# Optimization experiments

Measured on AMD Instinct MI355X. Metric: run time of the kernel, lower is better.

Reference implementation:

```python
import jax, jax.numpy as jnp
import numpy as np

B = 8
RESOLUTIONS = [65, 129, 257, 513, 1025]
NUM_POINTS = [0, 4096, 16384, 65536, 262144]
CLIP_MIN = -1e9
FINAL = 1025          # last resolution (both axes)
B_MIN, B_MAX = -1.0, 1.0
BALANCE = 0.5


def setup_inputs() -> dict:
    key = jax.random.key(0)
    k1, k2, k3, k4 = jax.random.split(key, 4)
    return {
        "w1": jax.random.normal(k1, (2, 256), jnp.float32),
        "b1": jax.random.normal(k2, (256,), jnp.float32),
        "w2": jax.random.normal(k3, (256, 1), jnp.float32),
        "b2": jax.random.normal(k4, (1,), jnp.float32),
    }


def _interp_bilinear_ac(x, H, W):
    """F.interpolate(..., mode='bilinear', align_corners=True). x: [B, C, h, w]."""
    b, c, h, w = x.shape
    ys = jnp.linspace(0.0, h - 1.0, H)
    xs = jnp.linspace(0.0, w - 1.0, W)
    y0 = jnp.floor(ys).astype(jnp.int32)
    y1 = jnp.minimum(y0 + 1, h - 1)
    wy = ys - y0
    x0 = jnp.floor(xs).astype(jnp.int32)
    x1 = jnp.minimum(x0 + 1, w - 1)
    wx = xs - x0
    # interpolate rows, then columns
    top = x[:, :, y0, :] * (1.0 - wy)[None, None, :, None] + x[:, :, y1, :] * wy[None, None, :, None]
    return top[:, :, :, x0] * (1.0 - wx) + top[:, :, :, x1] * wx


def _batch_eval(coords, w1, b1, w2, b2):
    """coords: [B, N, 2] in final-resolution pixel space (align_corners=False mapping).
    Returns occupancy [B, N] (C == 1)."""
    coords2d = coords / FINAL + 0.5 / FINAL                 # normalize to [0, 1]
    p = coords2d * (B_MAX - B_MIN) + B_MIN                  # [B, N, 2] in world coords
    h = jax.nn.relu(jnp.einsum('bnd,dh->bnh', p, w1) + b1)  # [B, N, 256]
    occ = jax.nn.sigmoid(jnp.einsum('bnh,ho->bno', h, w2) + b2)
    return occ[..., 0]


def reference(w1, b1, w2, b2):
    occ = None
    for i, res in enumerate(RESOLUTIONS):
        if i == 0:
            # init_coords: grid of res x res points spanning [0, FINAL-1]
            xs = jnp.linspace(0.0, FINAL - 1.0, res)
            gy, gx = jnp.meshgrid(xs, xs, indexing='ij')          # y rows, x cols
            coords = jnp.stack([gx.ravel(), gy.ravel()], axis=-1)  # [N, 2] (x, y)
            coords = jnp.broadcast_to(coords, (B, res * res, 2))
            o = _batch_eval(coords, w1, b1, w2, b2)               # [B, N]
            occ = o.reshape(B, 1, res, res)                       # [B, C, H, W]
        else:
            occ = _interp_bilinear_ac(occ, res, res)
            npt = NUM_POINTS[i]
            if npt <= 0:
                continue
            # uncertainty = -|occ - balance_value|
            unc = -jnp.abs(occ - BALANCE)                          # [B, 1, H, W]
            flat_unc = unc.reshape(B, res * res)
            scores, idx = jax.lax.top_k(flat_unc, npt)             # [B, npt]
            px = (idx % res).astype(jnp.float32)
            py = (idx // res).astype(jnp.float32)
            stride = (FINAL - 1.0) / (res - 1.0)
            coords = jnp.stack([px, py], axis=-1) * stride         # [B, npt, 2]
            new_vals = _batch_eval(coords, w1, b1, w2, b2)         # [B, npt]
            occ_flat = occ.reshape(B, res * res)
            old_vals = jnp.take_along_axis(occ_flat, idx, axis=1)
            vals = jnp.where(scores >= CLIP_MIN, new_vals, old_vals)
            occ_flat = jax.vmap(lambda o, i2, v: o.at[i2].set(v))(occ_flat, idx, vals)
            occ = occ_flat.reshape(B, 1, res, res)
    return occ
```

## Files before the change

### kernel.cpp

```cpp
#include <hip/hip_runtime.h>
#include <stdint.h>

#define HID 256
#define NMAXPIX (1025 * 1025)
#define NREP 8
#define NSEG 2048

#define HISTA_OFF 0
#define HISTB_OFF 16384
#define HISTC_OFF 32768
#define SCAL_OFF  40960
#define TIC_OFF   41024
#define STAGE_U32 43072

__device__ __forceinline__ unsigned long long aload64(const unsigned long long* p) {
    return __hip_atomic_load(p, __ATOMIC_RELAXED, __HIP_MEMORY_SCOPE_AGENT);
}
__device__ __forceinline__ void astore64(unsigned long long* p, unsigned long long v) {
    __hip_atomic_store(p, v, __ATOMIC_RELAXED, __HIP_MEMORY_SCOPE_AGENT);
}

__device__ __forceinline__ float mlp_eval4(float wx, float wy,
                                           const float4* __restrict__ w1x,
                                           const float4* __restrict__ w1y,
                                           const float4* __restrict__ vb1,
                                           const float4* __restrict__ vw2, float b2v) {
    const float C0 = (float)(0.5 / 1025.0);
    float px = (wx / 1025.0f + C0) * 2.0f - 1.0f;
    float py = (wy / 1025.0f + C0) * 2.0f - 1.0f;
    float a0 = 0.f, a1 = 0.f, a2 = 0.f, a3 = 0.f;
#pragma unroll 8
    for (int q = 0; q < HID / 4; ++q) {
        float4 a = w1x[q], b = w1y[q], c = vb1[q], d = vw2[q];
        float h0 = px * a.x + py * b.x + c.x;
        float h1 = px * a.y + py * b.y + c.y;
        float h2 = px * a.z + py * b.z + c.z;
        float h3 = px * a.w + py * b.w + c.w;
        h0 = h0 > 0.f ? h0 : 0.f;
        h1 = h1 > 0.f ? h1 : 0.f;
        h2 = h2 > 0.f ? h2 : 0.f;
        h3 = h3 > 0.f ? h3 : 0.f;
        a0 += h0 * d.x;
        a1 += h1 * d.y;
        a2 += h2 * d.z;
        a3 += h3 * d.w;
    }
    float x = ((a0 + a1) + (a2 + a3)) + b2v;
    float r;
    if (x >= 0.f) { r = 1.0f / (1.0f + expf(-x)); }
    else { float e = expf(x); r = e / (1.0f + e); }
    return r;
}

__device__ __forceinline__ uint32_t block_exscan_256(uint32_t v, volatile uint32_t* lds4) {
    int lane = threadIdx.x & 63, w = threadIdx.x >> 6;
    uint32_t inc = v;
#pragma unroll
    for (int d = 1; d < 64; d <<= 1) {
        uint32_t o = (uint32_t)__shfl_up((int)inc, d, 64);
        if (lane >= d) inc += o;
    }
    if (lane == 63) lds4[w] = inc;
    __syncthreads();
    uint32_t woff = 0;
    for (int i = 0; i < w; ++i) woff += lds4[i];
    return woff + inc - v;
}

__device__ void scan_generic(const uint32_t* __restrict__ hist, int NB, int nrep,
                             uint32_t rem_in, uint32_t prefix_in, int shift,
                             uint32_t* outp, uint32_t* outr,
                             volatile uint32_t* lds4, volatile uint32_t* ldspair) {
    int tid = threadIdx.x;
    int C = NB >> 8;
    int b0 = NB - (tid + 1) * C;
    uint32_t cnts[8];
#pragma unroll
    for (int k = 0; k < 8; ++k) cnts[k] = 0;
    for (int rep = 0; rep < nrep; ++rep) {
        const uint4* p = (const uint4*)(hist + (size_t)rep * NB + b0);
#pragma unroll
        for (int g = 0; g < 2; ++g) {
            if (g * 4 < C) {
                uint4 v = p[g];
                cnts[g * 4 + 0] += v.x;
                cnts[g * 4 + 1] += v.y;
                cnts[g * 4 + 2] += v.z;
                cnts[g * 4 + 3] += v.w;
            }
        }
    }
    uint32_t ssum = 0;
    for (int k = 0; k < C; ++k) ssum += cnts[k];
    uint32_t excl = block_exscan_256(ssum, lds4);
    uint32_t run = excl;
    for (int k = 0; k < C; ++k) {
        uint32_t c = cnts[C - 1 - k];
        if (rem_in > run && rem_in <= run + c) {
            ldspair[0] = (prefix_in << shift) | (uint32_t)(b0 + C - 1 - k);
            ldspair[1] = rem_in - run;
        }
        run += c;
    }
    __syncthreads();
    *outp = ldspair[0];
    *outr = ldspair[1];
}

__device__ __forceinline__ void hist_add(uint32_t* lh, uint32_t bin, bool act, int lane) {
    unsigned long long m = __ballot(act);
    if (m) {
        int leader = __ffsll(m) - 1;
        uint32_t lbin = (uint32_t)__shfl((int)bin, leader, 64);
        unsigned long long smk = __ballot(act && bin == lbin);
        if (smk == m) {
            if (lane == leader) atomicAdd(&lh[lbin], (uint32_t)__popcll(m));
        } else if (act) {
            atomicAdd(&lh[bin], 1u);
        }
    }
}

__device__ __forceinline__ float up2x(const float* __restrict__ in, int rp, int r, int n) {
    int i = n / r, j = n % r;
    int i2 = i >> 1, j2 = j >> 1;
    float v;
    if ((i & 1) == 0) {
        if ((j & 1) == 0) {
            v = in[i2 * rp + j2];
        } else {
            float a = in[i2 * rp + j2], b = in[i2 * rp + j2 + 1];
            v = a * 0.5f + b * 0.5f;
        }
    } else {
        if ((j & 1) == 0) {
            float a = in[i2 * rp + j2], b = in[(i2 + 1) * rp + j2];
            v = a * 0.5f + b * 0.5f;
        } else {
            float a = in[i2 * rp + j2],      c = in[i2 * rp + j2 + 1];
            float b = in[(i2 + 1) * rp + j2], d = in[(i2 + 1) * rp + j2 + 1];
            float t1 = a * 0.5f + b * 0.5f;
            float t2 = c * 0.5f + d * 0.5f;
            v = t1 * 0.5f + t2 * 0.5f;
        }
    }
    return v;
}

__device__ __forceinline__ uint32_t mkkey(float v) {
    float unc = -fabsf(v - 0.5f);
    uint32_t u = __float_as_uint(unc);
    return (u & 0x80000000u) ? ~u : (u | 0x80000000u);
}

__global__ __launch_bounds__(256) void k_eval0z(const float* __restrict__ w1, const float* __restrict__ b1,
                                                const float* __restrict__ w2, const float* __restrict__ b2,
                                                float* __restrict__ occ, uint32_t* __restrict__ zbuf, int zcount) {
    __shared__ alignas(16) float sw1[2 * HID];
    __shared__ alignas(16) float sb1[HID];
    __shared__ alignas(16) float sw2[HID];
    int tid = threadIdx.x;
    for (int i = tid; i < 2 * HID; i += 256) sw1[i] = w1[i];
    sb1[tid] = b1[tid];
    sw2[tid] = w2[tid];
    __syncthreads();
    int gtid = blockIdx.x * 256 + tid;
    int nthreads = gridDim.x * 256;
    for (int i = gtid; i < zcount; i += nthreads) zbuf[i] = 0;
    for (int n = gtid; n < 65 * 65; n += nthreads) {
        int i = n / 65, j = n % 65;
        occ[n] = mlp_eval4(16.0f * (float)j, 16.0f * (float)i,
                           (const float4*)sw1, (const float4*)(sw1 + HID),
                           (const float4*)sb1, (const float4*)sw2, b2[0]);
    }
}

__global__ __launch_bounds__(256) void k_upkey(const float* __restrict__ in, int rp,
                                               float* __restrict__ outg, int r, int nb, int bstride,
                                               uint32_t* __restrict__ keys,
                                               uint32_t* __restrict__ histA) {
    __shared__ uint32_t hist[2048];
    int tid = threadIdx.x;
    for (int k = tid; k < 2048; k += 256) hist[k] = 0;
    __syncthreads();
    int N = r * r;
    int lane = tid & 63;
    int gstride = gridDim.x * 256;
    for (int n0 = blockIdx.x * 256; n0 < N; n0 += gstride) {
        int n = n0 + tid;
        bool act = n < N;
        uint32_t key = 0;
        if (act) {
            float v = up2x(in, rp, r, n);
            for (int k = 0; k < nb; ++k) outg[(size_t)k * bstride + n] = v;
            key = mkkey(v);
            keys[n] = key;
        }
        hist_add(hist, key >> 21, act, lane);
    }
    __syncthreads();
    uint32_t* myrep = histA + (size_t)(blockIdx.x & (NREP - 1)) * 2048;
    for (int k = tid; k < 2048; k += 256) {
        uint32_t c = hist[k];
        if (c) atomicAdd(&myrep[k], c);
    }
}

__global__ __launch_bounds__(256) void k_histmid(const uint32_t* __restrict__ keys, int N,
                                                 const uint32_t* __restrict__ prevHist,
                                                 uint32_t* __restrict__ scal,
                                                 int useNpt, uint32_t npt, int scalInIdx, int shift,
                                                 int scalOutIdx,
                                                 int fshift, int bshift, uint32_t bmask,
                                                 uint32_t* __restrict__ outHist, int NBout) {
    __shared__ uint32_t lh[2048];
    __shared__ uint32_t lds4[4];
    __shared__ uint32_t ldspair[2];
    int tid = threadIdx.x, lane = tid & 63;
    uint32_t rem_in = useNpt ? npt : scal[scalInIdx + 1];
    uint32_t pfx_in = useNpt ? 0u  : scal[scalInIdx];
    uint32_t pfx, rem;
    scan_generic(prevHist, 2048, NREP, rem_in, pfx_in, shift, &pfx, &rem, lds4, ldspair);
    if (blockIdx.x == 0 && tid == 0) { scal[scalOutIdx] = pfx; scal[scalOutIdx + 1] = rem; }
    for (int k = tid; k < 2048; k += 256) lh[k] = 0;
    __syncthreads();
    int gstride = gridDim.x * 256;
    for (int base = blockIdx.x * 256; base < N; base += gstride) {
        int n = base + tid;
        bool inb = n < N;
        uint32_t key = inb ? keys[n] : 0u;
        bool flt = inb && ((key >> fshift) == pfx);
        uint32_t bin = (key >> bshift) & bmask;
        hist_add(lh, bin, flt, lane);
    }
    __syncthreads();
    uint32_t* myrep = outHist + (size_t)(blockIdx.x & (NREP - 1)) * NBout;
    for (int k = tid; k < NBout; k += 256) {
        uint32_t c = lh[k];
        if (c) atomicAdd(&myrep[k], c);
    }
}

__global__ __launch_bounds__(256, 2) void k_segselc(
        const uint32_t* __restrict__ keys, int N, int seglen,
        const uint32_t* __restrict__ histC,
        const uint32_t* __restrict__ scal,
        unsigned long long* __restrict__ tic64,
        uint32_t* __restrict__ selbuf) {
    __shared__ uint32_t lds4[4];
    __shared__ uint32_t ldspair[2];
    __shared__ uint32_t wtc[4], wgc[4];
    __shared__ uint32_t s_excl_t, s_excl_g;
    int tid = threadIdx.x, lane = tid & 63, w = tid >> 6;
    if (tid == 0) { s_excl_t = 0; s_excl_g = 0; }

    uint32_t rem2 = scal[3], pfx2 = scal[2];
    uint32_t K, t;
    scan_generic(histC, 1024, NREP, rem2, pfx2, 10, &K, &t, lds4, ldspair);

    int wv = blockIdx.x * 4 + w;
    int s0 = wv * seglen;
    int s1 = s0 + seglen; if (s1 > N) s1 = N;
    uint32_t tcnt = 0, gcnt2 = 0;
    for (int base = s0; base < s1; base += 64) {
        int n = base + lane;
        if (n < s1) {
            uint32_t key = keys[n];
            tcnt += (key == K) ? 1u : 0u;
            gcnt2 += (key > K) ? 1u : 0u;
        }
    }
#pragma unroll
    for (int d = 32; d; d >>= 1) {
        tcnt += (uint32_t)__shfl_down((int)tcnt, d, 64);
        gcnt2 += (uint32_t)__shfl_down((int)gcnt2, d, 64);
    }
    if (lane == 0) { wtc[w] = tcnt; wgc[w] = gcnt2; }
    __syncthreads();
    uint32_t agg_t = wtc[0] + wtc[1] + wtc[2] + wtc[3];
    uint32_t agg_g = wgc[0] + wgc[1] + wgc[2] + wgc[3];
    uint32_t intra_t = 0, intra_g = 0;
    for (int i = 0; i < w; ++i) { intra_t += wtc[i]; intra_g += wgc[i]; }

    if (tid == 0) {
        unsigned long long pay = ((unsigned long long)agg_t << 24) | (unsigned long long)agg_g;
        unsigned long long st = (blockIdx.x == 0) ? ((2ull << 62) | pay) : ((1ull << 62) | pay);
        astore64(&tic64[blockIdx.x], st);
    }
    if (blockIdx.x > 0 && w == 0) {
        uint32_t excl_t = 0, excl_g = 0;
        int b = (int)blockIdx.x - 1;
        for (;;) {
            int mine = b - lane;
            bool active = (mine >= 0);
            unsigned long long f = 0;
            if (active) {
                f = aload64(&tic64[mine]);
                int spins = 0;
                while ((f >> 62) == 0ull && spins < 1000) {
                    __builtin_amdgcn_s_sleep(2);
                    f = aload64(&tic64[mine]);
                    ++spins;
                }
                if ((f >> 62) == 0ull) {
                    int ms0 = mine * 4 * seglen;
                    int ms1 = ms0 + 4 * seglen; if (ms1 > N) ms1 = N;
                    uint32_t ct = 0, cg = 0;
                    for (int n2 = ms0; n2 < ms1; ++n2) {
                        uint32_t key = keys[n2];
                        ct += (key == K) ? 1u : 0u;
                        cg += (key > K) ? 1u : 0u;
                    }
                    f = (1ull << 62) | ((unsigned long long)ct << 24) | (unsigned long long)cg;
                }
            }
            unsigned long long incm = __ballot(active && (f >> 62) == 2ull);
            uint32_t vt, vg;
            bool done = (incm != 0ull);
            if (done) {
                int l2 = __ffsll(incm) - 1;
                vt = (lane <= l2) ? (uint32_t)((f >> 24) & 0xFFFFFFull) : 0u;
                vg = (lane <= l2) ? (uint32_t)(f & 0xFFFFFFull) : 0u;
            } else {
                vt = active ? (uint32_t)((f >> 24) & 0xFFFFFFull) : 0u;
                vg = active ? (uint32_t)(f & 0xFFFFFFull) : 0u;
            }
#pragma unroll
            for (int d = 32; d; d >>= 1) {
                vt += (uint32_t)__shfl_down((int)vt, d, 64);
                vg += (uint32_t)__shfl_down((int)vg, d, 64);
            }
            vt = (uint32_t)__shfl((int)vt, 0, 64);
            vg = (uint32_t)__shfl((int)vg, 0, 64);
            excl_t += vt;
            excl_g += vg;
            if (done) break;
            if (b < 64) break;
            b -= 64;
        }
        if (lane == 0) {
            unsigned long long pay = ((unsigned long long)(excl_t + agg_t) << 24)
                                   | (unsigned long long)(excl_g + agg_g);
            astore64(&tic64[blockIdx.x], (2ull << 62) | pay);
            s_excl_t = excl_t;
            s_excl_g = excl_g;
        }
    }
    __syncthreads();
    uint32_t tie_run = s_excl_t + intra_t;
    uint32_t gt_run  = s_excl_g + intra_g;

    unsigned long long lowmask = (lane == 63) ? ~0ull >> 1 : ((1ull << lane) - 1ull);
    for (int base = s0; base < s1; base += 64) {
        int n = base + lane;
        bool inb = n < s1;
        uint32_t key = inb ? keys[n] : 0u;
        bool gt = inb && (key > K);
        bool tie = inb && (key == K);
        unsigned long long tm = __ballot(tie);
        unsigned long long gm = __ballot(gt);
        uint32_t tie_before = tie_run + (uint32_t)__popcll(tm & lowmask);
        uint32_t gt_before  = gt_run + (uint32_t)__popcll(gm & lowmask);
        if (gt) {
            uint32_t tb = tie_before < t ? tie_before : t;
            selbuf[gt_before + tb] = (uint32_t)n;
        } else if (tie && tie_before < t) {
            selbuf[gt_before + tie_before] = (uint32_t)n;
        }
        tie_run += (uint32_t)__popcll(tm);
        gt_run  += (uint32_t)__popcll(gm);
    }
}

__global__ __launch_bounds__(256) void k_evalsel(const uint32_t* __restrict__ selbuf, int npt,
                                                 int r, float stride,
                                                 float* __restrict__ occ, int nb, int bstride,
                                                 const float* __restrict__ w1, const float* __restrict__ b1,
                                                 const float* __restrict__ w2, const float* __restrict__ b2) {
    __shared__ alignas(16) float sw1[2 * HID];
    __shared__ alignas(16) float sb1[HID];
    __shared__ alignas(16) float sw2[HID];
    int tid = threadIdx.x;
    for (int i = tid; i < 2 * HID; i += 256) sw1[i] = w1[i];
    sb1[tid] = b1[tid];
    sw2[tid] = w2[tid];
    __syncthreads();
    float vb2 = b2[0];
    const float4* w1x = (const float4*)sw1;
    const float4* w1y = (const float4*)(sw1 + HID);
    const float4* vb1 = (const float4*)sb1;
    const float4* vw2 = (const float4*)sw2;
    const float C0 = (float)(0.5 / 1025.0);
    int gs2 = gridDim.x * 512;
    for (int bb = blockIdx.x * 512; bb < npt; bb += gs2) {
        int i0 = bb + tid, i1 = bb + tid + 256;
        bool v0 = i0 < npt, v1 = i1 < npt;
        int nA = v0 ? (int)selbuf[i0] : 0;
        int nB = v1 ? (int)selbuf[i1] : 0;
        int iA = nA / r, jA = nA % r;
        int iB = nB / r, jB = nB % r;
        float pxA = ((stride * (float)jA) / 1025.0f + C0) * 2.0f - 1.0f;
        float pyA = ((stride * (float)iA) / 1025.0f + C0) * 2.0f - 1.0f;
        float pxB = ((stride * (float)jB) / 1025.0f + C0) * 2.0f - 1.0f;
        float pyB = ((stride * (float)iB) / 1025.0f + C0) * 2.0f - 1.0f;
        float4 A0 = {0, 0, 0, 0}, A1 = {0, 0, 0, 0};
#pragma unroll 4
        for (int q = 0; q < HID / 4; ++q) {
            float4 a = w1x[q], b = w1y[q], c = vb1[q], d = vw2[q];
            {
                float h0 = pxA * a.x + pyA * b.x + c.x;
                float h1 = pxA * a.y + pyA * b.y + c.y;
                float h2 = pxA * a.z + pyA * b.z + c.z;
                float h3 = pxA * a.w + pyA * b.w + c.w;
                h0 = h0 > 0.f ? h0 : 0.f;
                h1 = h1 > 0.f ? h1 : 0.f;
                h2 = h2 > 0.f ? h2 : 0.f;
                h3 = h3 > 0.f ? h3 : 0.f;
                A0.x += h0 * d.x; A0.y += h1 * d.y;
                A0.z += h2 * d.z; A0.w += h3 * d.w;
            }
            {
                float h0 = pxB * a.x + pyB * b.x + c.x;
                float h1 = pxB * a.y + pyB * b.y + c.y;
                float h2 = pxB * a.z + pyB * b.z + c.z;
                float h3 = pxB * a.w + pyB * b.w + c.w;
                h0 = h0 > 0.f ? h0 : 0.f;
                h1 = h1 > 0.f ? h1 : 0.f;
                h2 = h2 > 0.f ? h2 : 0.f;
                h3 = h3 > 0.f ? h3 : 0.f;
                A1.x += h0 * d.x; A1.y += h1 * d.y;
                A1.z += h2 * d.z; A1.w += h3 * d.w;
            }
        }
        if (v0) {
            float x = ((A0.x + A0.y) + (A0.z + A0.w)) + vb2;
            float rr;
            if (x >= 0.f) { rr = 1.0f / (1.0f + expf(-x)); }
            else { float e = expf(x); rr = e / (1.0f + e); }
            for (int k = 0; k < nb; ++k) occ[(size_t)k * bstride + nA] = rr;
        }
        if (v1) {
            float x = ((A1.x + A1.y) + (A1.z + A1.w)) + vb2;
            float rr;
            if (x >= 0.f) { rr = 1.0f / (1.0f + expf(-x)); }
            else { float e = expf(x); rr = e / (1.0f + e); }
            for (int k = 0; k < nb; ++k) occ[(size_t)k * bstride + nB] = rr;
        }
    }
}

__global__ __launch_bounds__(256) void k_bcast(const float* __restrict__ src, float* __restrict__ dst, int N) {
    int q = blockIdx.x * 256 + threadIdx.x;
    int n = q * 4;
    if (n + 3 < N) {
        float4 v = *(const float4*)(src + n);
#pragma unroll
        for (int k = 0; k < 8; ++k) *(float4*)(dst + (size_t)k * N + n) = v;
    } else if (n < N) {
        for (int m = n; m < N; ++m) {
            float v = src[m];
#pragma unroll
            for (int k = 0; k < 8; ++k) dst[(size_t)k * N + m] = v;
        }
    }
}

extern "C" void kernel_launch(void* const* d_in, const int* in_sizes, int n_in,
                              void* d_out, int out_size, void* d_ws, size_t ws_size,
                              hipStream_t stream) {
    const float* w1 = (const float*)d_in[0];
    const float* b1 = (const float*)d_in[1];
    const float* w2 = (const float*)d_in[2];
    const float* b2 = (const float*)d_in[3];
    float* out = (float*)d_out;

    const size_t A = (((size_t)NMAXPIX * 4) + 255) & ~(size_t)255;
    const size_t SMALL_BYTES = (size_t)4 * STAGE_U32 * 4;
    const size_t SELB_BYTES = ((size_t)262144 * 4 + 255) & ~(size_t)255;
    const size_t need = 3 * A + SMALL_BYTES + SELB_BYTES;

    int fused8 = (ws_size >= need);
    char* base = fused8 ? (char*)d_ws : (char*)d_out;
    float* buf0 = (float*)(base);
    float* buf1 = (float*)(base + A);
    uint32_t* keys = (uint32_t*)(base + 2 * A);
    uint32_t* smallb = (uint32_t*)(base + 3 * A);
    uint32_t* selbuf = (uint32_t*)(base + 3 * A + SMALL_BYTES);

    k_eval0z<<<dim3(512), dim3(256), 0, stream>>>(w1, b1, w2, b2, buf0, smallb, 4 * STAGE_U32);

    const int resA[5] = {65, 129, 257, 513, 1025};
    const int nptA[5] = {0, 4096, 16384, 65536, 262144};
    float* cur = buf0;
    float* nxt = buf1;
    for (int s = 1; s < 5; ++s) {
        int rp = resA[s - 1], r = resA[s];
        int N = r * r;
        uint32_t npt = (uint32_t)nptA[s];
        uint32_t* sm    = smallb + (size_t)(s - 1) * STAGE_U32;
        uint32_t* histA = sm + HISTA_OFF;
        uint32_t* histB = sm + HISTB_OFF;
        uint32_t* histC = sm + HISTC_OFF;
        uint32_t* scal  = sm + SCAL_OFF;
        uint32_t* tic   = sm + TIC_OFF;
        int nb1 = (N + 255) / 256;
        int nbu = nb1 < 1024 ? nb1 : 1024;
        int seglen = (N + NSEG - 1) / NSEG;
        float stride = 1024.0f / (float)(r - 1);

        int last = (s == 4);
        float* stage_out = (last && fused8) ? out : nxt;
        int nb = (last && fused8) ? 8 : 1;
        int bstride = (last && fused8) ? NMAXPIX : 0;
        int nbe = (int)((npt + 511) / 512); if (nbe > 512) nbe = 512;

        k_upkey<<<dim3(nbu), dim3(256), 0, stream>>>(cur, rp, stage_out, r, nb, bstride, keys, histA);
        k_histmid<<<dim3(512), dim3(256), 0, stream>>>(keys, N, histA, scal, 1, npt, 0, 0,
                                                       0, 21, 10, 0x7FFu, histB, 2048);
        k_histmid<<<dim3(512), dim3(256), 0, stream>>>(keys, N, histB, scal, 0, 0u, 0, 11,
                                                       2, 10, 0, 0x3FFu, histC, 1024);
        k_segselc<<<dim3(NSEG / 4), dim3(256), 0, stream>>>(keys, N, seglen, histC, scal,
                                                            (unsigned long long*)tic, selbuf);
        k_evalsel<<<dim3(nbe), dim3(256), 0, stream>>>(selbuf, (int)npt, r, stride,
                                                       stage_out, nb, bstride, w1, b1, w2, b2);
        if (!(last && fused8)) { float* tmp = cur; cur = nxt; nxt = tmp; }
    }
    if (!fused8) {
        k_bcast<<<dim3(((NMAXPIX + 3) / 4 + 255) / 256), dim3(256), 0, stream>>>(cur, out, NMAXPIX);
    }
}
```

Measured before the change: 229.8 us.

## Fuse selected-point MLP evaluation into segmented select kernel via sentinel polling

Merges the separate k_evalsel launch into k_segselc. Each block now waits, using polling with sleep, until its 1/512 slice of the selection buffer has been filled by other blocks. It then evaluates the MLP on those points directly. The selection buffer is pre-filled with sentinels and given a separate region per stage, so no reset is needed between stages. A slow fallback lets one wave recompute the missing indices if polling times out. The aim is to remove one kernel launch per stage, but it adds spin-wait latency, depends on inter-block forward progress, and raises LDS use in the fused kernel.

```diff
diff --git a/kernel.cpp b/kernel.cpp
--- a/kernel.cpp
+++ b/kernel.cpp
@@ -5,6 +5,7 @@
 #define NMAXPIX (1025 * 1025)
 #define NREP 8
 #define NSEG 2048
+#define SENT 0xFFFFFFFFu
 
 #define HISTA_OFF 0
 #define HISTB_OFF 16384
@@ -13,6 +14,14 @@
 #define TIC_OFF   41024
 #define STAGE_U32 43072
 
+#define SELB_U32 348160
+
+__device__ __forceinline__ uint32_t aload(const uint32_t* p) {
+    return __hip_atomic_load(p, __ATOMIC_RELAXED, __HIP_MEMORY_SCOPE_AGENT);
+}
+__device__ __forceinline__ void astore(uint32_t* p, uint32_t v) {
+    __hip_atomic_store(p, v, __ATOMIC_RELAXED, __HIP_MEMORY_SCOPE_AGENT);
+}
 __device__ __forceinline__ unsigned long long aload64(const unsigned long long* p) {
     return __hip_atomic_load(p, __ATOMIC_RELAXED, __HIP_MEMORY_SCOPE_AGENT);
 }
@@ -155,7 +164,8 @@
 
 __global__ __launch_bounds__(256) void k_eval0z(const float* __restrict__ w1, const float* __restrict__ b1,
                                                 const float* __restrict__ w2, const float* __restrict__ b2,
-                                                float* __restrict__ occ, uint32_t* __restrict__ zbuf, int zcount) {
+                                                float* __restrict__ occ, uint32_t* __restrict__ zbuf, int zcount,
+                                                uint32_t* __restrict__ selb, int scount) {
     __shared__ alignas(16) float sw1[2 * HID];
     __shared__ alignas(16) float sb1[HID];
     __shared__ alignas(16) float sw2[HID];
@@ -167,6 +177,7 @@
     int gtid = blockIdx.x * 256 + tid;
     int nthreads = gridDim.x * 256;
     for (int i = gtid; i < zcount; i += nthreads) zbuf[i] = 0;
+    for (int i = gtid; i < scount; i += nthreads) selb[i] = SENT;
     for (int n = gtid; n < 65 * 65; n += nthreads) {
         int i = n / 65, j = n % 65;
         occ[n] = mlp_eval4(16.0f * (float)j, 16.0f * (float)i,
@@ -246,13 +257,27 @@
         const uint32_t* __restrict__ histC,
         const uint32_t* __restrict__ scal,
         unsigned long long* __restrict__ tic64,
-        uint32_t* __restrict__ selbuf) {
+        uint32_t* __restrict__ selbuf, uint32_t npt,
+        int r, float stride,
+        float* __restrict__ occ, int nb, int bstride,
+        const float* __restrict__ w1, const float* __restrict__ b1,
+        const float* __restrict__ w2, const float* __restrict__ b2) {
+    __shared__ alignas(16) float sw1[2 * HID];
+    __shared__ alignas(16) float sb1[HID];
+    __shared__ alignas(16) float sw2[HID];
+    __shared__ uint32_t lslice[512];
     __shared__ uint32_t lds4[4];
     __shared__ uint32_t ldspair[2];
     __shared__ uint32_t wtc[4], wgc[4];
     __shared__ uint32_t s_excl_t, s_excl_g;
+    __shared__ uint32_t miss;
     int tid = threadIdx.x, lane = tid & 63, w = tid >> 6;
-    if (tid == 0) { s_excl_t = 0; s_excl_g = 0; }
+    unsigned long long lowmask = (lane == 63) ? ~0ull >> 1 : ((1ull << lane) - 1ull);
+    for (int i = tid; i < 2 * HID; i += 256) sw1[i] = w1[i];
+    sb1[tid] = b1[tid];
+    sw2[tid] = w2[tid];
+    if (tid == 0) { s_excl_t = 0; s_excl_g = 0; miss = 0; }
+    float vb2 = b2[0];
 
     uint32_t rem2 = scal[3], pfx2 = scal[2];
     uint32_t K, t;
@@ -350,7 +375,6 @@
     uint32_t tie_run = s_excl_t + intra_t;
     uint32_t gt_run  = s_excl_g + intra_g;
 
-    unsigned long long lowmask = (lane == 63) ? ~0ull >> 1 : ((1ull << lane) - 1ull);
     for (int base = s0; base < s1; base += 64) {
         int n = base + lane;
         bool inb = n < s1;
@@ -363,40 +387,62 @@
         uint32_t gt_before  = gt_run + (uint32_t)__popcll(gm & lowmask);
         if (gt) {
             uint32_t tb = tie_before < t ? tie_before : t;
-            selbuf[gt_before + tb] = (uint32_t)n;
+            astore(&selbuf[gt_before + tb], (uint32_t)n);
         } else if (tie && tie_before < t) {
-            selbuf[gt_before + tie_before] = (uint32_t)n;
+            astore(&selbuf[gt_before + tie_before], (uint32_t)n);
         }
         tie_run += (uint32_t)__popcll(tm);
         gt_run  += (uint32_t)__popcll(gm);
     }
-}
-
-__global__ __launch_bounds__(256) void k_evalsel(const uint32_t* __restrict__ selbuf, int npt,
-                                                 int r, float stride,
-                                                 float* __restrict__ occ, int nb, int bstride,
-                                                 const float* __restrict__ w1, const float* __restrict__ b1,
-                                                 const float* __restrict__ w2, const float* __restrict__ b2) {
-    __shared__ alignas(16) float sw1[2 * HID];
-    __shared__ alignas(16) float sb1[HID];
-    __shared__ alignas(16) float sw2[HID];
-    int tid = threadIdx.x;
-    for (int i = tid; i < 2 * HID; i += 256) sw1[i] = w1[i];
-    sb1[tid] = b1[tid];
-    sw2[tid] = w2[tid];
-    __syncthreads();
-    float vb2 = b2[0];
+    __syncthreads();
+
+    int per = (int)(npt >> 9);
+    int lo = (int)blockIdx.x * per;
+    for (int i = tid; i < per; i += 256) {
+        uint32_t n = aload(&selbuf[lo + i]);
+        int sp = 0;
+        while (n == SENT && sp < 1200) {
+            __builtin_amdgcn_s_sleep(2);
+            n = aload(&selbuf[lo + i]);
+            ++sp;
+        }
+        lslice[i] = n;
+        if (n == SENT) miss = 1;
+    }
+    __syncthreads();
+    if (miss && w == 0) {
+        uint32_t tr = 0, gr = 0;
+        for (int base = 0; base < N; base += 64) {
+            int n2 = base + lane;
+            bool inb = n2 < N;
+            uint32_t key = inb ? keys[n2] : 0u;
+            bool gt = inb && (key > K);
+            bool tie = inb && (key == K);
+            unsigned long long tm = __ballot(tie);
+            unsigned long long gm = __ballot(gt);
+            uint32_t tb = tr + (uint32_t)__popcll(tm & lowmask);
+            uint32_t gb = gr + (uint32_t)__popcll(gm & lowmask);
+            int dest = -1;
+            if (gt) { uint32_t x = tb < t ? tb : t; dest = (int)(gb + x); }
+            else if (tie && tb < t) dest = (int)(gb + tb);
+            if (dest >= lo && dest < lo + per && lslice[dest - lo] == SENT)
+                lslice[dest - lo] = (uint32_t)n2;
+            tr += (uint32_t)__popcll(tm);
+            gr += (uint32_t)__popcll(gm);
+        }
+    }
+    __syncthreads();
+
     const float4* w1x = (const float4*)sw1;
     const float4* w1y = (const float4*)(sw1 + HID);
     const float4* vb1 = (const float4*)sb1;
     const float4* vw2 = (const float4*)sw2;
     const float C0 = (float)(0.5 / 1025.0);
-    int gs2 = gridDim.x * 512;
-    for (int bb = blockIdx.x * 512; bb < npt; bb += gs2) {
+    for (int bb = 0; bb < per; bb += 512) {
         int i0 = bb + tid, i1 = bb + tid + 256;
-        bool v0 = i0 < npt, v1 = i1 < npt;
-        int nA = v0 ? (int)selbuf[i0] : 0;
-        int nB = v1 ? (int)selbuf[i1] : 0;
+        bool v0 = i0 < per, v1 = i1 < per;
+        int nA = v0 ? (int)lslice[i0] : 0;
+        int nB = v1 ? (int)lslice[i1] : 0;
         int iA = nA / r, jA = nA % r;
         int iB = nB / r, jB = nB % r;
         float pxA = ((stride * (float)jA) / 1025.0f + C0) * 2.0f - 1.0f;
@@ -476,7 +522,7 @@
 
     const size_t A = (((size_t)NMAXPIX * 4) + 255) & ~(size_t)255;
     const size_t SMALL_BYTES = (size_t)4 * STAGE_U32 * 4;
-    const size_t SELB_BYTES = ((size_t)262144 * 4 + 255) & ~(size_t)255;
+    const size_t SELB_BYTES = ((size_t)SELB_U32 * 4 + 255) & ~(size_t)255;
     const size_t need = 3 * A + SMALL_BYTES + SELB_BYTES;
 
     int fused8 = (ws_size >= need);
@@ -487,10 +533,12 @@
     uint32_t* smallb = (uint32_t*)(base + 3 * A);
     uint32_t* selbuf = (uint32_t*)(base + 3 * A + SMALL_BYTES);
 
-    k_eval0z<<<dim3(512), dim3(256), 0, stream>>>(w1, b1, w2, b2, buf0, smallb, 4 * STAGE_U32);
+    k_eval0z<<<dim3(512), dim3(256), 0, stream>>>(w1, b1, w2, b2, buf0, smallb, 4 * STAGE_U32,
+                                                  selbuf, SELB_U32);
 
     const int resA[5] = {65, 129, 257, 513, 1025};
     const int nptA[5] = {0, 4096, 16384, 65536, 262144};
+    const int selOff[5] = {0, 0, 4096, 20480, 86016};
     float* cur = buf0;
     float* nxt = buf1;
     for (int s = 1; s < 5; ++s) {
@@ -512,7 +560,6 @@
         float* stage_out = (last && fused8) ? out : nxt;
         int nb = (last && fused8) ? 8 : 1;
         int bstride = (last && fused8) ? NMAXPIX : 0;
-        int nbe = (int)((npt + 511) / 512); if (nbe > 512) nbe = 512;
 
         k_upkey<<<dim3(nbu), dim3(256), 0, stream>>>(cur, rp, stage_out, r, nb, bstride, keys, histA);
         k_histmid<<<dim3(512), dim3(256), 0, stream>>>(keys, N, histA, scal, 1, npt, 0, 0,
@@ -520,9 +567,10 @@
         k_histmid<<<dim3(512), dim3(256), 0, stream>>>(keys, N, histB, scal, 0, 0u, 0, 11,
                                                        2, 10, 0, 0x3FFu, histC, 1024);
         k_segselc<<<dim3(NSEG / 4), dim3(256), 0, stream>>>(keys, N, seglen, histC, scal,
-                                                            (unsigned long long*)tic, selbuf);
-        k_evalsel<<<dim3(nbe), dim3(256), 0, stream>>>(selbuf, (int)npt, r, stride,
-                                                       stage_out, nb, bstride, w1, b1, w2, b2);
+                                                            (unsigned long long*)tic,
+                                                            selbuf + selOff[s], npt,
+                                                            r, stride, stage_out, nb, bstride,
+                                                            w1, b1, w2, b2);
         if (!(last && fused8)) { float* tmp = cur; cur = nxt; nxt = tmp; }
     }
     if (!fused8) {
```

New measurement: 231.9 us. About the same (+0.9%).
